# Kernel tuning notes

Measured on AMD Instinct MI355X. Metric: run time of the kernel, lower is better.

The kernel has to match this reference:

```python
import jax, jax.numpy as jnp
import numpy as np

N_NODES = 100000
N_EDGES = 1600000
F_IN = 256
EMB = 16  # conv1 out = 2*EMB = 32, conv2 out = EMB


def setup_inputs() -> dict:
    key = jax.random.key(0)
    k1, k2, k3, k4, k5, k6, k7 = jax.random.split(key, 7)
    x = jax.random.normal(k1, (N_NODES, F_IN), dtype=jnp.float32)
    edge_index = jax.random.randint(k2, (2, N_EDGES), 0, N_NODES, dtype=jnp.int64)
    edge_weight = jax.random.uniform(k3, (N_EDGES,), dtype=jnp.float32)
    # GCNConv params: glorot-ish weights, zero bias (materialized as params)
    s1 = 1.0 / np.sqrt(F_IN)
    s2 = 1.0 / np.sqrt(2 * EMB)
    W1 = jax.random.uniform(k4, (F_IN, 2 * EMB), minval=-s1, maxval=s1, dtype=jnp.float32)
    b1 = jnp.zeros((2 * EMB,), dtype=jnp.float32)
    W2 = jax.random.uniform(k5, (2 * EMB, EMB), minval=-s2, maxval=s2, dtype=jnp.float32)
    b2 = jnp.zeros((EMB,), dtype=jnp.float32)
    return {"x": x, "edge_index": edge_index, "edge_weight": edge_weight,
            "W1": W1, "b1": b1, "W2": W2, "b2": b2}


def _gcn_norm(edge_index, edge_weight, num_nodes, dtype):
    # PyG gcn_norm with add_self_loops=True, fill_value=1.0
    row, col = edge_index[0], edge_index[1]
    loop = jnp.arange(num_nodes)
    row_a = jnp.concatenate([row, loop])
    col_a = jnp.concatenate([col, loop])
    w_a = jnp.concatenate([edge_weight, jnp.ones((num_nodes,), dtype=dtype)])
    deg = jax.ops.segment_sum(w_a, col_a, num_segments=num_nodes)
    dinv = jnp.where(deg > 0, jax.lax.rsqrt(deg), jnp.zeros_like(deg))
    norm = dinv[row_a] * w_a * dinv[col_a]
    return row_a, col_a, norm


def _gcn_conv(x, W, b, row, col, norm, num_nodes):
    h = x @ W                                  # [N, d_out] dense projection
    msg = norm[:, None] * h[row]               # gather + edge scale, [E+N, d_out]
    out = jax.ops.segment_sum(msg, col, num_segments=num_nodes)  # scatter-add
    return out + b


def reference(x, edge_index, edge_weight, W1, b1, W2, b2):
    n = x.shape[0]
    row, col, norm = _gcn_norm(edge_index, edge_weight, n, x.dtype)
    h = jax.nn.relu(_gcn_conv(x, W1, b1, row, col, norm, n))
    return _gcn_conv(h, W2, b2, row, col, norm, n)
```

## Files before the change

kernel.cpp:

```cpp
#include <hip/hip_runtime.h>
#include <hip/hip_bf16.h>

#define NN   100000
#define NE   1600000
#define FIN  256
#define HID  32
#define OUTD 16
#define NBLK ((NN + 255) / 256)
#define GEMM_BLOCKS ((NN + 127) / 128)
#define CNT_BLOCKS  ((NE + 255) / 256)
#define FUSE_BLOCKS (GEMM_BLOCKS + CNT_BLOCKS)

#define OFF_FLAG    0
#define OFF_DEGPACK 64
#define OFF_DINV    (OFF_DEGPACK + 2*NN)
#define OFF_RANK    (OFF_DINV + NN)
#define OFF_BSUM    (OFF_RANK + NE)
#define OFF_BOFF    (OFF_BSUM + 512)
#define OFF_ROWPTR  (OFF_BOFF + 512)
#define OFF_CSR     (OFF_ROWPTR + NN + 32)
#define OFF_H1      (OFF_CSR + 2*NE)
#define OFF_P2      (OFF_H1 + NN*HID)

#define PACK_SHIFT 40
#define PACK_MASK  ((1ull << PACK_SHIFT) - 1ull)
#define FP_SCALE   16777216.0f
#define FP_INV     (1.0f / 16777216.0f)

__device__ __forceinline__ float bf2f(unsigned short u) {
  union { unsigned int i; float f; } v; v.i = ((unsigned int)u) << 16; return v.f;
}
__device__ __forceinline__ unsigned short f2bf(float f) {
  union { float f; unsigned int i; } v; v.f = f;
  unsigned int x = v.i;
  return (unsigned short)((x + 0x7fffu + ((x >> 16) & 1u)) >> 16);
}
__device__ __forceinline__ int eidx(const int* __restrict__ ei, long long pos, int is64) {
  return is64 ? ei[2 * pos] : ei[pos];
}
__device__ __forceinline__ float ldf(const void* p, long long i, int isf32) {
  return isf32 ? ((const float*)p)[i] : bf2f(((const unsigned short*)p)[i]);
}

__global__ __launch_bounds__(256) void detect_zero_kernel(const int* __restrict__ ei,
    const unsigned short* __restrict__ xu, int* __restrict__ flags,
    float* __restrict__ zp, int zn) {
  int b = blockIdx.x;
  if (b == 0) {
    __shared__ int any, cnt;
    if (threadIdx.x == 0) { any = 0; cnt = 0; }
    __syncthreads();
    int local = 0, c = 0;
    for (int i = threadIdx.x; i < 2048; i += 256) local |= ei[2 * i + 1];
    for (int i = threadIdx.x; i < 1024; i += 256) {
      unsigned int e = (xu[2 * i] >> 7) & 0xFF;
      c += (e < 100 || e > 140) ? 1 : 0;
    }
    if (local) atomicOr(&any, 1);
    atomicAdd(&cnt, c);
    __syncthreads();
    if (threadIdx.x == 0) {
      flags[0] = (any == 0) ? 1 : 0;
      flags[1] = (cnt > 100) ? 1 : 0;
    }
  } else {
    int stride = (gridDim.x - 1) * 256;
    for (int i = (b - 1) * 256 + threadIdx.x; i < zn; i += stride) zp[i] = 0.f;
  }
}

__global__ __launch_bounds__(256) void count_gemm_kernel(const int* __restrict__ ei,
    const void* __restrict__ ew, unsigned long long* __restrict__ degpack,
    int* __restrict__ rank, const void* __restrict__ x,
    const void* __restrict__ W1, float* __restrict__ h1,
    const int* __restrict__ flags) {
  __shared__ float wlds[FIN][HID];
  __shared__ float xs[32][132];
  int b = blockIdx.x;
  int t = threadIdx.x;
  bool is_gemm = ((b % 9) == 0) && (b / 9) < GEMM_BLOCKS;

  if (!is_gemm) {
    int cid = b - 1 - b / 9;
    int e = cid * 256 + t;
    if (e >= NE) return;
    int c = eidx(ei, (long long)NE + e, flags[0]);
    float w = ldf(ew, e, flags[1]);
    unsigned long long inc = (1ull << PACK_SHIFT)
                           | (unsigned long long)(w * FP_SCALE + 0.5f);
    unsigned long long old = atomicAdd(degpack + c, inc);
    rank[e] = (int)(old >> PACK_SHIFT);
    return;
  }

  int rb = (b / 9) * 128;
  int isf32 = flags[1];

  if (isf32) {
    const float* wrow = (const float*)W1 + t * HID;
    #pragma unroll
    for (int jj = 0; jj < HID; jj += 4)
      *(float4*)&wlds[t][jj] = *((const float4*)(wrow + jj));
  } else {
    const unsigned short* wrow = (const unsigned short*)W1 + t * HID;
    #pragma unroll
    for (int jj = 0; jj < HID; jj += 8) {
      uint4 pk = *((const uint4*)(wrow + jj));
      const unsigned short* pu = (const unsigned short*)&pk;
      #pragma unroll
      for (int q = 0; q < 8; q++) wlds[t][jj + q] = bf2f(pu[q]);
    }
  }

  int j0 = (t & 15) * 2;
  int r0 = (t >> 4) * 8;
  float acc[8][2];
  #pragma unroll
  for (int i = 0; i < 8; i++) { acc[i][0] = 0.f; acc[i][1] = 0.f; }

  for (int kc = 0; kc < FIN; kc += 32) {
    __syncthreads();
    {
      int rr = t >> 1;
      int kk0 = (t & 1) * 16;
      int grow = rb + rr;
      if (grow < NN) {
        if (isf32) {
          const float* xp = (const float*)x + (long long)grow * FIN + kc + kk0;
          #pragma unroll
          for (int q4 = 0; q4 < 4; q4++) {
            float4 p = ((const float4*)xp)[q4];
            xs[kk0 + q4 * 4 + 0][rr] = p.x;
            xs[kk0 + q4 * 4 + 1][rr] = p.y;
            xs[kk0 + q4 * 4 + 2][rr] = p.z;
            xs[kk0 + q4 * 4 + 3][rr] = p.w;
          }
        } else {
          const unsigned short* xp = (const unsigned short*)x + (long long)grow * FIN + kc + kk0;
          uint4 p0 = ((const uint4*)xp)[0];
          uint4 p1 = ((const uint4*)xp)[1];
          const unsigned short* pu = (const unsigned short*)&p0;
          #pragma unroll
          for (int q = 0; q < 8; q++) xs[kk0 + q][rr] = bf2f(pu[q]);
          pu = (const unsigned short*)&p1;
          #pragma unroll
          for (int q = 0; q < 8; q++) xs[kk0 + 8 + q][rr] = bf2f(pu[q]);
        }
      } else {
        #pragma unroll
        for (int q = 0; q < 16; q++) xs[kk0 + q][rr] = 0.f;
      }
    }
    __syncthreads();
    #pragma unroll 8
    for (int kk = 0; kk < 32; kk++) {
      float w0 = wlds[kc + kk][j0];
      float w1 = wlds[kc + kk][j0 + 1];
      const float4* xr = (const float4*)&xs[kk][r0];
      float4 xa = xr[0], xb = xr[1];
      float xv[8] = {xa.x, xa.y, xa.z, xa.w, xb.x, xb.y, xb.z, xb.w};
      #pragma unroll
      for (int i = 0; i < 8; i++) {
        acc[i][0] = fmaf(xv[i], w0, acc[i][0]);
        acc[i][1] = fmaf(xv[i], w1, acc[i][1]);
      }
    }
  }
  #pragma unroll
  for (int i = 0; i < 8; i++) {
    int grow = rb + r0 + i;
    if (grow < NN) {
      float2 v; v.x = acc[i][0]; v.y = acc[i][1];
      *((float2*)(h1 + (long long)grow * HID + j0)) = v;
    }
  }
}

__global__ __launch_bounds__(256) void dinv_scansum_kernel(
    const unsigned long long* __restrict__ degpack, float* __restrict__ dinv,
    int* __restrict__ bsum) {
  int b = blockIdx.x;
  if (b < NBLK) {
    __shared__ int s[256];
    int i = b * 256 + threadIdx.x;
    s[threadIdx.x] = (i < NN) ? (int)(degpack[i] >> PACK_SHIFT) : 0;
    __syncthreads();
    for (int off = 128; off > 0; off >>= 1) {
      if (threadIdx.x < off) s[threadIdx.x] += s[threadIdx.x + off];
      __syncthreads();
    }
    if (threadIdx.x == 0) bsum[b] = s[0];
  } else {
    int i = (b - NBLK) * 256 + threadIdx.x;
    if (i >= NN) return;
    float d = (float)(degpack[i] & PACK_MASK) * FP_INV + 1.0f;
    dinv[i] = (d > 0.f) ? rsqrtf(d) : 0.f;
  }
}

__global__ __launch_bounds__(512) void scan_offs_kernel(const int* __restrict__ bsum,
                                                        int* __restrict__ boff) {
  __shared__ int a[512];
  int t = threadIdx.x;
  int orig = (t < NBLK) ? bsum[t] : 0;
  a[t] = orig;
  __syncthreads();
  for (int off = 1; off < 512; off <<= 1) {
    int v = a[t] + ((t >= off) ? a[t - off] : 0);
    __syncthreads();
    a[t] = v;
    __syncthreads();
  }
  if (t < NBLK) boff[t] = a[t] - orig;
}

__global__ __launch_bounds__(256) void scan_write_kernel(const unsigned long long* __restrict__ degpack,
    const int* __restrict__ boff, int* __restrict__ rowptr) {
  __shared__ int a[256];
  int t = threadIdx.x;
  int i = blockIdx.x * 256 + t;
  int orig = (i < NN) ? (int)(degpack[i] >> PACK_SHIFT) : 0;
  a[t] = orig;
  __syncthreads();
  for (int off = 1; off < 256; off <<= 1) {
    int v = a[t] + ((t >= off) ? a[t - off] : 0);
    __syncthreads();
    a[t] = v;
    __syncthreads();
  }
  if (i < NN) rowptr[i] = boff[blockIdx.x] + a[t] - orig;
  if (blockIdx.x == 0 && t == 0) rowptr[NN] = NE;
}

__global__ __launch_bounds__(256) void fill_csr_kernel(const int* __restrict__ ei,
    const void* __restrict__ ew, const float* __restrict__ dinv,
    const int* __restrict__ rowptr, const int* __restrict__ rank,
    int2* __restrict__ csr, const int* __restrict__ flags) {
  int e = blockIdx.x * 256 + threadIdx.x;
  if (e >= NE) return;
  int is64 = flags[0];
  int r = eidx(ei, e, is64);
  int c = eidx(ei, (long long)NE + e, is64);
  float nw = dinv[r] * ldf(ew, e, flags[1]) * dinv[c];
  int pos = rowptr[c] + rank[e];
  int2 pr; pr.x = r; pr.y = __float_as_int(nw);
  csr[pos] = pr;
}

__global__ __launch_bounds__(256) void gather1_kernel(const float* __restrict__ h1,
    const float* __restrict__ dinv, const int* __restrict__ rowptr,
    const int2* __restrict__ csr, const void* __restrict__ b1,
    const void* __restrict__ W2, float* __restrict__ p2,
    const int* __restrict__ flags) {
  __shared__ float w2lds[HID * OUTD];
  __shared__ float b1l[HID];
  __shared__ float tl[8][HID + 1];
  int t = threadIdx.x;
  int isf32 = flags[1];
  w2lds[2 * t]     = ldf(W2, 2 * t, isf32);
  w2lds[2 * t + 1] = ldf(W2, 2 * t + 1, isf32);
  if (t < HID) b1l[t] = ldf(b1, t, isf32);
  __syncthreads();

  int nl = t >> 5;
  int j  = t & 31;
  int node = blockIdx.x * 8 + nl;
  if (node < NN) {
    int k0 = rowptr[node], k1 = rowptr[node + 1];
    float acc = 0.f;
    int k = k0;
    for (; k + 8 <= k1; k += 8) {
      int2 q0 = csr[k];     int2 q1 = csr[k + 1];
      int2 q2 = csr[k + 2]; int2 q3 = csr[k + 3];
      int2 q4 = csr[k + 4]; int2 q5 = csr[k + 5];
      int2 q6 = csr[k + 6]; int2 q7 = csr[k + 7];
      float v0 = h1[q0.x * HID + j]; float v1 = h1[q1.x * HID + j];
      float v2 = h1[q2.x * HID + j]; float v3 = h1[q3.x * HID + j];
      float v4 = h1[q4.x * HID + j]; float v5 = h1[q5.x * HID + j];
      float v6 = h1[q6.x * HID + j]; float v7 = h1[q7.x * HID + j];
      acc = fmaf(__int_as_float(q0.y), v0, acc);
      acc = fmaf(__int_as_float(q1.y), v1, acc);
      acc = fmaf(__int_as_float(q2.y), v2, acc);
      acc = fmaf(__int_as_float(q3.y), v3, acc);
      acc = fmaf(__int_as_float(q4.y), v4, acc);
      acc = fmaf(__int_as_float(q5.y), v5, acc);
      acc = fmaf(__int_as_float(q6.y), v6, acc);
      acc = fmaf(__int_as_float(q7.y), v7, acc);
    }
    for (; k + 4 <= k1; k += 4) {
      int2 q0 = csr[k];     int2 q1 = csr[k + 1];
      int2 q2 = csr[k + 2]; int2 q3 = csr[k + 3];
      float v0 = h1[q0.x * HID + j]; float v1 = h1[q1.x * HID + j];
      float v2 = h1[q2.x * HID + j]; float v3 = h1[q3.x * HID + j];
      acc = fmaf(__int_as_float(q0.y), v0, acc);
      acc = fmaf(__int_as_float(q1.y), v1, acc);
      acc = fmaf(__int_as_float(q2.y), v2, acc);
      acc = fmaf(__int_as_float(q3.y), v3, acc);
    }
    for (; k < k1; k++) {
      int2 pr = csr[k];
      acc = fmaf(__int_as_float(pr.y), h1[pr.x * HID + j], acc);
    }
    float di = dinv[node];
    acc = fmaf(di * di, h1[node * HID + j], acc);
    acc += b1l[j];
    tl[nl][j] = fmaxf(acc, 0.f);
  }
  __syncthreads();
  int m = t & 31;
  if (node < NN && m < OUTD) {
    float s = 0.f;
    #pragma unroll
    for (int k = 0; k < HID; k++) s = fmaf(tl[nl][k], w2lds[k * OUTD + m], s);
    p2[node * OUTD + m] = s;
  }
}

__global__ __launch_bounds__(256) void gather2_kernel(const float* __restrict__ p2,
    const float* __restrict__ dinv, const int* __restrict__ rowptr,
    const int2* __restrict__ csr, const void* __restrict__ b2,
    void* __restrict__ out, const int* __restrict__ flags) {
  __shared__ float b2l[OUTD];
  int t = threadIdx.x;
  int isf32 = flags[1];
  if (t < OUTD) b2l[t] = ldf(b2, t, isf32);
  __syncthreads();

  int nl = t >> 4;
  int m  = t & 15;
  int node = blockIdx.x * 16 + nl;
  if (node >= NN) return;
  int k0 = rowptr[node], k1 = rowptr[node + 1];
  float acc = 0.f;
  int k = k0;
  for (; k + 8 <= k1; k += 8) {
    int2 q0 = csr[k];     int2 q1 = csr[k + 1];
    int2 q2 = csr[k + 2]; int2 q3 = csr[k + 3];
    int2 q4 = csr[k + 4]; int2 q5 = csr[k + 5];
    int2 q6 = csr[k + 6]; int2 q7 = csr[k + 7];
    float v0 = p2[q0.x * OUTD + m]; float v1 = p2[q1.x * OUTD + m];
    float v2 = p2[q2.x * OUTD + m]; float v3 = p2[q3.x * OUTD + m];
    float v4 = p2[q4.x * OUTD + m]; float v5 = p2[q5.x * OUTD + m];
    float v6 = p2[q6.x * OUTD + m]; float v7 = p2[q7.x * OUTD + m];
    acc = fmaf(__int_as_float(q0.y), v0, acc);
    acc = fmaf(__int_as_float(q1.y), v1, acc);
    acc = fmaf(__int_as_float(q2.y), v2, acc);
    acc = fmaf(__int_as_float(q3.y), v3, acc);
    acc = fmaf(__int_as_float(q4.y), v4, acc);
    acc = fmaf(__int_as_float(q5.y), v5, acc);
    acc = fmaf(__int_as_float(q6.y), v6, acc);
    acc = fmaf(__int_as_float(q7.y), v7, acc);
  }
  for (; k + 4 <= k1; k += 4) {
    int2 q0 = csr[k];     int2 q1 = csr[k + 1];
    int2 q2 = csr[k + 2]; int2 q3 = csr[k + 3];
    float v0 = p2[q0.x * OUTD + m]; float v1 = p2[q1.x * OUTD + m];
    float v2 = p2[q2.x * OUTD + m]; float v3 = p2[q3.x * OUTD + m];
    acc = fmaf(__int_as_float(q0.y), v0, acc);
    acc = fmaf(__int_as_float(q1.y), v1, acc);
    acc = fmaf(__int_as_float(q2.y), v2, acc);
    acc = fmaf(__int_as_float(q3.y), v3, acc);
  }
  for (; k < k1; k++) {
    int2 pr = csr[k];
    acc = fmaf(__int_as_float(pr.y), p2[pr.x * OUTD + m], acc);
  }
  float di = dinv[node];
  acc = fmaf(di * di, p2[node * OUTD + m], acc);
  acc += b2l[m];
  int oidx = node * OUTD + m;
  if (isf32) ((float*)out)[oidx] = acc;
  else       ((unsigned short*)out)[oidx] = f2bf(acc);
}

extern "C" void kernel_launch(void* const* d_in, const int* in_sizes, int n_in,
                              void* d_out, int out_size, void* d_ws, size_t ws_size,
                              hipStream_t stream) {
  const void* x  = d_in[0];
  const int* ei  = (const int*)d_in[1];
  const void* ew = d_in[2];
  const void* W1 = d_in[3];
  const void* b1 = d_in[4];
  const void* W2 = d_in[5];
  const void* b2 = d_in[6];
  float* ws = (float*)d_ws;
  int* wsi = (int*)d_ws;
  unsigned long long* degpack = (unsigned long long*)(wsi + OFF_DEGPACK);

  detect_zero_kernel<<<dim3(513), dim3(256), 0, stream>>>(ei, (const unsigned short*)x,
      wsi + OFF_FLAG, ws + OFF_DEGPACK, 2 * NN);
  count_gemm_kernel<<<dim3(FUSE_BLOCKS), dim3(256), 0, stream>>>(ei, ew, degpack,
      wsi + OFF_RANK, x, W1, ws + OFF_H1, wsi + OFF_FLAG);
  dinv_scansum_kernel<<<dim3(2 * NBLK), dim3(256), 0, stream>>>(degpack, ws + OFF_DINV, wsi + OFF_BSUM);
  scan_offs_kernel<<<dim3(1), dim3(512), 0, stream>>>(wsi + OFF_BSUM, wsi + OFF_BOFF);
  scan_write_kernel<<<dim3(NBLK), dim3(256), 0, stream>>>(degpack, wsi + OFF_BOFF, wsi + OFF_ROWPTR);
  fill_csr_kernel<<<dim3((NE + 255) / 256), dim3(256), 0, stream>>>(ei, ew, ws + OFF_DINV, wsi + OFF_ROWPTR, wsi + OFF_RANK, (int2*)(wsi + OFF_CSR), wsi + OFF_FLAG);
  gather1_kernel<<<dim3((NN + 7) / 8), dim3(256), 0, stream>>>(ws + OFF_H1, ws + OFF_DINV, wsi + OFF_ROWPTR, (const int2*)(wsi + OFF_CSR), b1, W2, ws + OFF_P2, wsi + OFF_FLAG);
  gather2_kernel<<<dim3((NN + 15) / 16), dim3(256), 0, stream>>>(ws + OFF_P2, ws + OFF_DINV, wsi + OFF_ROWPTR, (const int2*)(wsi + OFF_CSR), b2, d_out, wsi + OFF_FLAG);
}
```

Before: 363.7 us.

## Build CSR via two-level bucket sort instead of global atomics

Replaces the global per-node 64-bit atomic degree counting and rank array with a histogram over 256-node buckets, column scans, and a scatter into bucket-ordered temp storage. A per-bucket build kernel then computes degrees, dinv, rowptr and the final CSR with shared-memory atomics. Normalization is refactored so h1 and p2 are pre-scaled by dinv and the edge weight is stored raw, which removes the dinv gathers during CSR fill. This trades contended global atomics and the extra rank pass for more kernels and an extra pass over temp records. Within-node edge order now depends on shared-atomic ordering, so results can differ slightly between runs.

```diff
diff --git a/kernel.cpp b/kernel.cpp
--- a/kernel.cpp
+++ b/kernel.cpp
@@ -6,26 +6,22 @@
 #define FIN  256
 #define HID  32
 #define OUTD 16
-#define NBLK ((NN + 255) / 256)
+
+#define NB    391
+#define NHB   256
+#define EPB   (NE / NHB)
 #define GEMM_BLOCKS ((NN + 127) / 128)
-#define CNT_BLOCKS  ((NE + 255) / 256)
-#define FUSE_BLOCKS (GEMM_BLOCKS + CNT_BLOCKS)
 
 #define OFF_FLAG    0
-#define OFF_DEGPACK 64
-#define OFF_DINV    (OFF_DEGPACK + 2*NN)
-#define OFF_RANK    (OFF_DINV + NN)
-#define OFF_BSUM    (OFF_RANK + NE)
-#define OFF_BOFF    (OFF_BSUM + 512)
-#define OFF_ROWPTR  (OFF_BOFF + 512)
-#define OFF_CSR     (OFF_ROWPTR + NN + 32)
+#define OFF_HIST    64
+#define OFF_TOT     (OFF_HIST + NHB*NB)
+#define OFF_BASE    (OFF_TOT + 392)
+#define OFF_ROWPTR  (OFF_BASE + 392)
+#define OFF_DINV    (OFF_ROWPTR + NN + 32)
+#define OFF_TEMP    (OFF_DINV + NN + 16)
+#define OFF_CSR     (OFF_TEMP + 2*NE)
 #define OFF_H1      (OFF_CSR + 2*NE)
-#define OFF_P2      (OFF_H1 + NN*HID)
-
-#define PACK_SHIFT 40
-#define PACK_MASK  ((1ull << PACK_SHIFT) - 1ull)
-#define FP_SCALE   16777216.0f
-#define FP_INV     (1.0f / 16777216.0f)
+#define OFF_P2S     OFF_TEMP
 
 __device__ __forceinline__ float bf2f(unsigned short u) {
   union { unsigned int i; float f; } v; v.i = ((unsigned int)u) << 16; return v.f;
@@ -42,58 +38,110 @@
   return isf32 ? ((const float*)p)[i] : bf2f(((const unsigned short*)p)[i]);
 }
 
-__global__ __launch_bounds__(256) void detect_zero_kernel(const int* __restrict__ ei,
-    const unsigned short* __restrict__ xu, int* __restrict__ flags,
-    float* __restrict__ zp, int zn) {
-  int b = blockIdx.x;
-  if (b == 0) {
-    __shared__ int any, cnt;
-    if (threadIdx.x == 0) { any = 0; cnt = 0; }
-    __syncthreads();
-    int local = 0, c = 0;
-    for (int i = threadIdx.x; i < 2048; i += 256) local |= ei[2 * i + 1];
-    for (int i = threadIdx.x; i < 1024; i += 256) {
-      unsigned int e = (xu[2 * i] >> 7) & 0xFF;
-      c += (e < 100 || e > 140) ? 1 : 0;
-    }
-    if (local) atomicOr(&any, 1);
-    atomicAdd(&cnt, c);
-    __syncthreads();
-    if (threadIdx.x == 0) {
-      flags[0] = (any == 0) ? 1 : 0;
-      flags[1] = (cnt > 100) ? 1 : 0;
-    }
-  } else {
-    int stride = (gridDim.x - 1) * 256;
-    for (int i = (b - 1) * 256 + threadIdx.x; i < zn; i += stride) zp[i] = 0.f;
-  }
-}
-
-__global__ __launch_bounds__(256) void count_gemm_kernel(const int* __restrict__ ei,
-    const void* __restrict__ ew, unsigned long long* __restrict__ degpack,
-    int* __restrict__ rank, const void* __restrict__ x,
-    const void* __restrict__ W1, float* __restrict__ h1,
-    const int* __restrict__ flags) {
+__global__ __launch_bounds__(256) void detect_kernel(const int* __restrict__ ei,
+    const unsigned short* __restrict__ xu, int* __restrict__ flags) {
+  __shared__ int any, cnt;
+  if (threadIdx.x == 0) { any = 0; cnt = 0; }
+  __syncthreads();
+  int local = 0, c = 0;
+  for (int i = threadIdx.x; i < 2048; i += 256) local |= ei[2 * i + 1];
+  for (int i = threadIdx.x; i < 1024; i += 256) {
+    unsigned int e = (xu[2 * i] >> 7) & 0xFF;
+    c += (e < 100 || e > 140) ? 1 : 0;
+  }
+  if (local) atomicOr(&any, 1);
+  atomicAdd(&cnt, c);
+  __syncthreads();
+  if (threadIdx.x == 0) {
+    flags[0] = (any == 0) ? 1 : 0;
+    flags[1] = (cnt > 100) ? 1 : 0;
+  }
+}
+
+__global__ __launch_bounds__(256) void hist_kernel(const int* __restrict__ ei,
+    int* __restrict__ hist, const int* __restrict__ flags) {
+  __shared__ int lh[NB];
+  int b = blockIdx.x, t = threadIdx.x;
+  for (int i = t; i < NB; i += 256) lh[i] = 0;
+  __syncthreads();
+  int is64 = flags[0];
+  long long e0 = (long long)b * EPB;
+  for (int i = t; i < EPB; i += 256) {
+    int dst = eidx(ei, (long long)NE + e0 + i, is64);
+    atomicAdd(&lh[dst >> 8], 1);
+  }
+  __syncthreads();
+  for (int i = t; i < NB; i += 256) hist[b * NB + i] = lh[i];
+}
+
+__global__ __launch_bounds__(256) void scan_cols_kernel(int* __restrict__ hist,
+                                                        int* __restrict__ tot) {
+  __shared__ int a[256];
+  int b = blockIdx.x, t = threadIdx.x;
+  int orig = hist[t * NB + b];
+  a[t] = orig;
+  __syncthreads();
+  for (int off = 1; off < 256; off <<= 1) {
+    int v = a[t] + ((t >= off) ? a[t - off] : 0);
+    __syncthreads(); a[t] = v; __syncthreads();
+  }
+  hist[t * NB + b] = a[t] - orig;
+  if (t == 255) tot[b] = a[255];
+}
+
+__global__ __launch_bounds__(512) void scan_base_kernel(const int* __restrict__ tot,
+    int* __restrict__ base, int* __restrict__ rowptr) {
+  __shared__ int a[512];
+  int t = threadIdx.x;
+  int orig = (t < NB) ? tot[t] : 0;
+  a[t] = orig;
+  __syncthreads();
+  for (int off = 1; off < 512; off <<= 1) {
+    int v = a[t] + ((t >= off) ? a[t - off] : 0);
+    __syncthreads(); a[t] = v; __syncthreads();
+  }
+  if (t < NB) base[t] = a[t] - orig;
+  if (t == 0) { base[NB] = NE; rowptr[NN] = NE; }
+}
+
+__global__ __launch_bounds__(256) void scatter_gemm_kernel(const int* __restrict__ ei,
+    const void* __restrict__ ew, const int* __restrict__ hist,
+    const int* __restrict__ base, int2* __restrict__ temp,
+    const void* __restrict__ x, const void* __restrict__ W1,
+    float* __restrict__ h1, const int* __restrict__ flags) {
   __shared__ float wlds[FIN][HID];
   __shared__ float xs[32][132];
-  int b = blockIdx.x;
-  int t = threadIdx.x;
-  bool is_gemm = ((b % 9) == 0) && (b / 9) < GEMM_BLOCKS;
-
-  if (!is_gemm) {
-    int cid = b - 1 - b / 9;
-    int e = cid * 256 + t;
-    if (e >= NE) return;
-    int c = eidx(ei, (long long)NE + e, flags[0]);
-    float w = ldf(ew, e, flags[1]);
-    unsigned long long inc = (1ull << PACK_SHIFT)
-                           | (unsigned long long)(w * FP_SCALE + 0.5f);
-    unsigned long long old = atomicAdd(degpack + c, inc);
-    rank[e] = (int)(old >> PACK_SHIFT);
+  int b = blockIdx.x, t = threadIdx.x;
+  int r4 = b & 3;
+
+  if (r4 == 3) {
+    int scid = b >> 2;
+    if (scid >= NHB) return;
+    int* lbase = (int*)wlds;
+    int* lcnt  = ((int*)wlds) + 512;
+    for (int i = t; i < NB; i += 256) {
+      lbase[i] = base[i] + hist[scid * NB + i];
+      lcnt[i] = 0;
+    }
+    __syncthreads();
+    int is64 = flags[0], isf32 = flags[1];
+    long long e0 = (long long)scid * EPB;
+    for (int i = t; i < EPB; i += 256) {
+      long long e = e0 + i;
+      int src = eidx(ei, e, is64);
+      int dst = eidx(ei, (long long)NE + e, is64);
+      float w = ldf(ew, e, isf32);
+      int bk = dst >> 8;
+      int r = atomicAdd(&lcnt[bk], 1);
+      int2 rec; rec.x = src | ((dst & 255) << 17); rec.y = __float_as_int(w);
+      temp[lbase[bk] + r] = rec;
+    }
     return;
   }
 
-  int rb = (b / 9) * 128;
+  int gid = (b >> 2) * 3 + r4;
+  if (gid >= GEMM_BLOCKS) return;
+  int rb = gid * 128;
   int isf32 = flags[1];
 
   if (isf32) {
@@ -176,85 +224,66 @@
   }
 }
 
-__global__ __launch_bounds__(256) void dinv_scansum_kernel(
-    const unsigned long long* __restrict__ degpack, float* __restrict__ dinv,
-    int* __restrict__ bsum) {
-  int b = blockIdx.x;
-  if (b < NBLK) {
-    __shared__ int s[256];
-    int i = b * 256 + threadIdx.x;
-    s[threadIdx.x] = (i < NN) ? (int)(degpack[i] >> PACK_SHIFT) : 0;
-    __syncthreads();
-    for (int off = 128; off > 0; off >>= 1) {
-      if (threadIdx.x < off) s[threadIdx.x] += s[threadIdx.x + off];
-      __syncthreads();
-    }
-    if (threadIdx.x == 0) bsum[b] = s[0];
-  } else {
-    int i = (b - NBLK) * 256 + threadIdx.x;
-    if (i >= NN) return;
-    float d = (float)(degpack[i] & PACK_MASK) * FP_INV + 1.0f;
-    dinv[i] = (d > 0.f) ? rsqrtf(d) : 0.f;
-  }
-}
-
-__global__ __launch_bounds__(512) void scan_offs_kernel(const int* __restrict__ bsum,
-                                                        int* __restrict__ boff) {
-  __shared__ int a[512];
-  int t = threadIdx.x;
-  int orig = (t < NBLK) ? bsum[t] : 0;
-  a[t] = orig;
-  __syncthreads();
-  for (int off = 1; off < 512; off <<= 1) {
-    int v = a[t] + ((t >= off) ? a[t - off] : 0);
-    __syncthreads();
-    a[t] = v;
-    __syncthreads();
-  }
-  if (t < NBLK) boff[t] = a[t] - orig;
-}
-
-__global__ __launch_bounds__(256) void scan_write_kernel(const unsigned long long* __restrict__ degpack,
-    const int* __restrict__ boff, int* __restrict__ rowptr) {
-  __shared__ int a[256];
-  int t = threadIdx.x;
-  int i = blockIdx.x * 256 + t;
-  int orig = (i < NN) ? (int)(degpack[i] >> PACK_SHIFT) : 0;
-  a[t] = orig;
+__global__ __launch_bounds__(256) void build_kernel(const int2* __restrict__ temp,
+    const int* __restrict__ base, int* __restrict__ rowptr,
+    float* __restrict__ dinv, int2* __restrict__ csr, float* __restrict__ h1) {
+  __shared__ int   cnt[256];
+  __shared__ float wsum[256];
+  __shared__ int   roff[256];
+  __shared__ float dnv[256];
+  __shared__ int   sbuf[256];
+  int b = blockIdx.x, t = threadIdx.x;
+  cnt[t] = 0; wsum[t] = 0.f;
+  __syncthreads();
+  int e0 = base[b], e1 = base[b + 1];
+  for (int e = e0 + t; e < e1; e += 256) {
+    int2 rec = temp[e];
+    int dl = (rec.x >> 17) & 255;
+    atomicAdd(&cnt[dl], 1);
+    atomicAdd(&wsum[dl], __int_as_float(rec.y));
+  }
+  __syncthreads();
+  int orig = cnt[t];
+  sbuf[t] = orig;
   __syncthreads();
   for (int off = 1; off < 256; off <<= 1) {
-    int v = a[t] + ((t >= off) ? a[t - off] : 0);
-    __syncthreads();
-    a[t] = v;
-    __syncthreads();
-  }
-  if (i < NN) rowptr[i] = boff[blockIdx.x] + a[t] - orig;
-  if (blockIdx.x == 0 && t == 0) rowptr[NN] = NE;
-}
-
-__global__ __launch_bounds__(256) void fill_csr_kernel(const int* __restrict__ ei,
-    const void* __restrict__ ew, const float* __restrict__ dinv,
-    const int* __restrict__ rowptr, const int* __restrict__ rank,
-    int2* __restrict__ csr, const int* __restrict__ flags) {
-  int e = blockIdx.x * 256 + threadIdx.x;
-  if (e >= NE) return;
-  int is64 = flags[0];
-  int r = eidx(ei, e, is64);
-  int c = eidx(ei, (long long)NE + e, is64);
-  float nw = dinv[r] * ldf(ew, e, flags[1]) * dinv[c];
-  int pos = rowptr[c] + rank[e];
-  int2 pr; pr.x = r; pr.y = __float_as_int(nw);
-  csr[pos] = pr;
+    int v = sbuf[t] + ((t >= off) ? sbuf[t - off] : 0);
+    __syncthreads(); sbuf[t] = v; __syncthreads();
+  }
+  roff[t] = sbuf[t] - orig;
+  int nb0 = b * 256;
+  int node = nb0 + t;
+  if (node < NN) {
+    rowptr[node] = e0 + roff[t];
+    float dv = rsqrtf(wsum[t] + 1.0f);
+    dinv[node] = dv;
+    dnv[t] = dv;
+  }
+  cnt[t] = 0;
+  __syncthreads();
+  int nn = NN - nb0; if (nn > 256) nn = 256;
+  for (int idx = t; idx < nn * HID; idx += 256) {
+    int nl = idx >> 5, j = idx & 31;
+    h1[(nb0 + nl) * HID + j] *= dnv[nl];
+  }
+  for (int e = e0 + t; e < e1; e += 256) {
+    int2 rec = temp[e];
+    int dl = (rec.x >> 17) & 255;
+    int r = atomicAdd(&cnt[dl], 1);
+    int2 o; o.x = rec.x & 0x1FFFF; o.y = rec.y;
+    csr[e0 + roff[dl] + r] = o;
+  }
 }
 
 __global__ __launch_bounds__(256) void gather1_kernel(const float* __restrict__ h1,
     const float* __restrict__ dinv, const int* __restrict__ rowptr,
     const int2* __restrict__ csr, const void* __restrict__ b1,
-    const void* __restrict__ W2, float* __restrict__ p2,
+    const void* __restrict__ W2, float* __restrict__ p2s,
     const int* __restrict__ flags) {
   __shared__ float w2lds[HID * OUTD];
   __shared__ float b1l[HID];
   __shared__ float tl[8][HID + 1];
+  __shared__ float dloc[8];
   int t = threadIdx.x;
   int isf32 = flags[1];
   w2lds[2 * t]     = ldf(W2, 2 * t, isf32);
@@ -301,10 +330,10 @@
       int2 pr = csr[k];
       acc = fmaf(__int_as_float(pr.y), h1[pr.x * HID + j], acc);
     }
+    acc += h1[node * HID + j];
     float di = dinv[node];
-    acc = fmaf(di * di, h1[node * HID + j], acc);
-    acc += b1l[j];
-    tl[nl][j] = fmaxf(acc, 0.f);
+    if (j == 0) dloc[nl] = di;
+    tl[nl][j] = fmaxf(fmaf(di, acc, b1l[j]), 0.f);
   }
   __syncthreads();
   int m = t & 31;
@@ -312,11 +341,11 @@
     float s = 0.f;
     #pragma unroll
     for (int k = 0; k < HID; k++) s = fmaf(tl[nl][k], w2lds[k * OUTD + m], s);
-    p2[node * OUTD + m] = s;
-  }
-}
-
-__global__ __launch_bounds__(256) void gather2_kernel(const float* __restrict__ p2,
+    p2s[node * OUTD + m] = dloc[nl] * s;
+  }
+}
+
+__global__ __launch_bounds__(256) void gather2_kernel(const float* __restrict__ p2s,
     const float* __restrict__ dinv, const int* __restrict__ rowptr,
     const int2* __restrict__ csr, const void* __restrict__ b2,
     void* __restrict__ out, const int* __restrict__ flags) {
@@ -338,10 +367,10 @@
     int2 q2 = csr[k + 2]; int2 q3 = csr[k + 3];
     int2 q4 = csr[k + 4]; int2 q5 = csr[k + 5];
     int2 q6 = csr[k + 6]; int2 q7 = csr[k + 7];
-    float v0 = p2[q0.x * OUTD + m]; float v1 = p2[q1.x * OUTD + m];
-    float v2 = p2[q2.x * OUTD + m]; float v3 = p2[q3.x * OUTD + m];
-    float v4 = p2[q4.x * OUTD + m]; float v5 = p2[q5.x * OUTD + m];
-    float v6 = p2[q6.x * OUTD + m]; float v7 = p2[q7.x * OUTD + m];
+    float v0 = p2s[q0.x * OUTD + m]; float v1 = p2s[q1.x * OUTD + m];
+    float v2 = p2s[q2.x * OUTD + m]; float v3 = p2s[q3.x * OUTD + m];
+    float v4 = p2s[q4.x * OUTD + m]; float v5 = p2s[q5.x * OUTD + m];
+    float v6 = p2s[q6.x * OUTD + m]; float v7 = p2s[q7.x * OUTD + m];
     acc = fmaf(__int_as_float(q0.y), v0, acc);
     acc = fmaf(__int_as_float(q1.y), v1, acc);
     acc = fmaf(__int_as_float(q2.y), v2, acc);
@@ -354,8 +383,8 @@
   for (; k + 4 <= k1; k += 4) {
     int2 q0 = csr[k];     int2 q1 = csr[k + 1];
     int2 q2 = csr[k + 2]; int2 q3 = csr[k + 3];
-    float v0 = p2[q0.x * OUTD + m]; float v1 = p2[q1.x * OUTD + m];
-    float v2 = p2[q2.x * OUTD + m]; float v3 = p2[q3.x * OUTD + m];
+    float v0 = p2s[q0.x * OUTD + m]; float v1 = p2s[q1.x * OUTD + m];
+    float v2 = p2s[q2.x * OUTD + m]; float v3 = p2s[q3.x * OUTD + m];
     acc = fmaf(__int_as_float(q0.y), v0, acc);
     acc = fmaf(__int_as_float(q1.y), v1, acc);
     acc = fmaf(__int_as_float(q2.y), v2, acc);
@@ -363,14 +392,13 @@
   }
   for (; k < k1; k++) {
     int2 pr = csr[k];
-    acc = fmaf(__int_as_float(pr.y), p2[pr.x * OUTD + m], acc);
-  }
-  float di = dinv[node];
-  acc = fmaf(di * di, p2[node * OUTD + m], acc);
-  acc += b2l[m];
+    acc = fmaf(__int_as_float(pr.y), p2s[pr.x * OUTD + m], acc);
+  }
+  acc += p2s[node * OUTD + m];
+  float v = fmaf(dinv[node], acc, b2l[m]);
   int oidx = node * OUTD + m;
-  if (isf32) ((float*)out)[oidx] = acc;
-  else       ((unsigned short*)out)[oidx] = f2bf(acc);
+  if (isf32) ((float*)out)[oidx] = v;
+  else       ((unsigned short*)out)[oidx] = f2bf(v);
 }
 
 extern "C" void kernel_launch(void* const* d_in, const int* in_sizes, int n_in,
@@ -385,16 +413,17 @@
   const void* b2 = d_in[6];
   float* ws = (float*)d_ws;
   int* wsi = (int*)d_ws;
-  unsigned long long* degpack = (unsigned long long*)(wsi + OFF_DEGPACK);
-
-  detect_zero_kernel<<<dim3(513), dim3(256), 0, stream>>>(ei, (const unsigned short*)x,
-      wsi + OFF_FLAG, ws + OFF_DEGPACK, 2 * NN);
-  count_gemm_kernel<<<dim3(FUSE_BLOCKS), dim3(256), 0, stream>>>(ei, ew, degpack,
-      wsi + OFF_RANK, x, W1, ws + OFF_H1, wsi + OFF_FLAG);
-  dinv_scansum_kernel<<<dim3(2 * NBLK), dim3(256), 0, stream>>>(degpack, ws + OFF_DINV, wsi + OFF_BSUM);
-  scan_offs_kernel<<<dim3(1), dim3(512), 0, stream>>>(wsi + OFF_BSUM, wsi + OFF_BOFF);
-  scan_write_kernel<<<dim3(NBLK), dim3(256), 0, stream>>>(degpack, wsi + OFF_BOFF, wsi + OFF_ROWPTR);
-  fill_csr_kernel<<<dim3((NE + 255) / 256), dim3(256), 0, stream>>>(ei, ew, ws + OFF_DINV, wsi + OFF_ROWPTR, wsi + OFF_RANK, (int2*)(wsi + OFF_CSR), wsi + OFF_FLAG);
-  gather1_kernel<<<dim3((NN + 7) / 8), dim3(256), 0, stream>>>(ws + OFF_H1, ws + OFF_DINV, wsi + OFF_ROWPTR, (const int2*)(wsi + OFF_CSR), b1, W2, ws + OFF_P2, wsi + OFF_FLAG);
-  gather2_kernel<<<dim3((NN + 15) / 16), dim3(256), 0, stream>>>(ws + OFF_P2, ws + OFF_DINV, wsi + OFF_ROWPTR, (const int2*)(wsi + OFF_CSR), b2, d_out, wsi + OFF_FLAG);
-}
+
+  detect_kernel<<<dim3(1), dim3(256), 0, stream>>>(ei, (const unsigned short*)x, wsi + OFF_FLAG);
+  hist_kernel<<<dim3(NHB), dim3(256), 0, stream>>>(ei, wsi + OFF_HIST, wsi + OFF_FLAG);
+  scan_cols_kernel<<<dim3(NB), dim3(256), 0, stream>>>(wsi + OFF_HIST, wsi + OFF_TOT);
+  scan_base_kernel<<<dim3(1), dim3(512), 0, stream>>>(wsi + OFF_TOT, wsi + OFF_BASE, wsi + OFF_ROWPTR);
+  scatter_gemm_kernel<<<dim3(1042), dim3(256), 0, stream>>>(ei, ew, wsi + OFF_HIST,
+      wsi + OFF_BASE, (int2*)(wsi + OFF_TEMP), x, W1, ws + OFF_H1, wsi + OFF_FLAG);
+  build_kernel<<<dim3(NB), dim3(256), 0, stream>>>((const int2*)(wsi + OFF_TEMP),
+      wsi + OFF_BASE, wsi + OFF_ROWPTR, ws + OFF_DINV, (int2*)(wsi + OFF_CSR), ws + OFF_H1);
+  gather1_kernel<<<dim3((NN + 7) / 8), dim3(256), 0, stream>>>(ws + OFF_H1, ws + OFF_DINV,
+      wsi + OFF_ROWPTR, (const int2*)(wsi + OFF_CSR), b1, W2, ws + OFF_P2S, wsi + OFF_FLAG);
+  gather2_kernel<<<dim3((NN + 15) / 16), dim3(256), 0, stream>>>(ws + OFF_P2S, ws + OFF_DINV,
+      wsi + OFF_ROWPTR, (const int2*)(wsi + OFF_CSR), b2, d_out, wsi + OFF_FLAG);
+}
```

New measurement: 371.1 us. +2.0%, slower.
